# Performance work log

Measured on AMD Instinct MI355X. Metric: run time of the kernel, lower is better.

Reference implementation:

```python
import jax, jax.numpy as jnp
import numpy as np

BETA = 0.25  # commitment cost


def setup_inputs() -> dict:
    key = jax.random.key(0)
    k1, k2 = jax.random.split(key)
    B, C, T = 16, 256, 1024      # batch, emb_dim channels, sequence length
    N_EMB = 8192                 # codebook size
    z = jax.random.normal(k1, (B, C, T), dtype=jnp.float32)
    # original init: uniform(-1/n_emb, 1/n_emb); scale a normal similarly small
    emb = jax.random.normal(k2, (N_EMB, C), dtype=jnp.float32) * (1.0 / N_EMB)
    return {"z": z, "emb": emb}


def reference(z, emb):
    sg = jax.lax.stop_gradient
    # [B, C, T] -> [B, T, C]
    zt = jnp.transpose(z, (0, 2, 1))
    B, T, C = zt.shape
    zf = zt.reshape(-1, C)  # [B*T, C]
    # squared euclidean distances: ||z||^2 + ||e||^2 - 2 z.e  -> [B*T, N]
    d = (jnp.sum(zf * zf, axis=1, keepdims=True)
         + jnp.sum(emb * emb, axis=1)
         - 2.0 * jnp.einsum('bd,nd->bn', zf, emb))
    idx = jnp.argmin(d, axis=-1)               # [B*T]
    z_q = emb[idx].reshape(B, T, C)            # [B, T, C]
    loss = (BETA * jnp.mean((sg(z_q) - zt) ** 2)
            + jnp.mean((z_q - sg(zt)) ** 2))
    # straight-through estimator
    z_q = zt + sg(z_q - zt)
    z_q = jnp.transpose(z_q, (0, 2, 1))        # back to [B, C, T]
    return z_q, loss, idx
```

## Files before the change

kernel.cpp:

```cpp
#include <hip/hip_runtime.h>


#define C_    256
#define T_    1024
#define M_    16384
#define N_    8192

#define OUT_ZQ   0
#define OUT_LOSS 4194304
#define OUT_IDX  4194305

#define WS_SZ    0
#define WS_SE    16384
#define WS_PART  24576
#define MIN_OFF  131072u
#define FB_OFF   8519680u
#define WS_NEED  16908288u
#define O_I1     24576
#define O_I2     40960
#define O_PART   73728

typedef __attribute__((ext_vector_type(8))) short bf16x8;
typedef __attribute__((ext_vector_type(4))) float f32x4;
typedef unsigned long long ull;

__device__ __forceinline__ unsigned short f2b(float f) {
    unsigned u = __float_as_uint(f);
    return (unsigned short)((u + 0x7FFFu + ((u >> 16) & 1u)) >> 16);
}
__device__ __forceinline__ float b2f(unsigned short u) {
    return __uint_as_float(((unsigned)u) << 16);
}

__global__ __launch_bounds__(256) void vq_sums(const float* __restrict__ z,
                                               const float* __restrict__ emb,
                                               float* __restrict__ ws) {
    int gid = blockIdx.x * 256 + threadIdx.x;
    if (gid < M_) {
        int b = gid >> 10, t = gid & (T_ - 1);
        const float* zp = z + (size_t)b * C_ * T_ + t;
        float blk[2];
#pragma unroll
        for (int h = 0; h < 2; ++h) {
            float r[8];
#pragma unroll
            for (int j = 0; j < 8; ++j) {
                float v = zp[(size_t)(h * 128 + j) * T_];
                r[j] = __fmul_rn(v, v);
            }
            for (int i = 8; i < 128; i += 8)
#pragma unroll
                for (int j = 0; j < 8; ++j) {
                    float v = zp[(size_t)(h * 128 + i + j) * T_];
                    r[j] = __fadd_rn(r[j], __fmul_rn(v, v));
                }
            blk[h] = __fadd_rn(__fadd_rn(__fadd_rn(r[0], r[1]), __fadd_rn(r[2], r[3])),
                               __fadd_rn(__fadd_rn(r[4], r[5]), __fadd_rn(r[6], r[7])));
        }
        ws[WS_SZ + gid] = __fadd_rn(blk[0], blk[1]);
    } else if (gid < M_ + N_) {
        int n = gid - M_;
        const float* ep = emb + (size_t)n * C_;
        float blk[2];
#pragma unroll
        for (int h = 0; h < 2; ++h) {
            float r[8];
#pragma unroll
            for (int j = 0; j < 8; ++j) {
                float v = ep[h * 128 + j];
                r[j] = __fmul_rn(v, v);
            }
            for (int i = 8; i < 128; i += 8)
#pragma unroll
                for (int j = 0; j < 8; ++j) {
                    float v = ep[h * 128 + i + j];
                    r[j] = __fadd_rn(r[j], __fmul_rn(v, v));
                }
            blk[h] = __fadd_rn(__fadd_rn(__fadd_rn(r[0], r[1]), __fadd_rn(r[2], r[3])),
                               __fadd_rn(__fadd_rn(r[4], r[5]), __fadd_rn(r[6], r[7])));
        }
        ws[WS_SE + n] = __fadd_rn(blk[0], blk[1]);
    }
}

__global__ __launch_bounds__(256) void vq_prep_b(const float* __restrict__ emb,
                                                 char* __restrict__ fb) {
    int gid = blockIdx.x * 256 + threadIdx.x;
    int n = gid >> 5, kg = gid & 31;
    const float* ep = emb + (size_t)n * C_ + kg * 8;
    unsigned hi[8], lo[8];
#pragma unroll
    for (int j = 0; j < 8; ++j) {
        float v = ep[j];
        unsigned short h = f2b(v);
        hi[j] = h;
        lo[j] = f2b(v - b2f(h));
    }
    int nt = n >> 4, kt = kg >> 2, lane = (kg & 3) * 16 + (n & 15);
    size_t base = ((size_t)((nt * 8 + kt) * 2) << 10) + (lane << 4);
    uint4 hv = {hi[0] | (hi[1] << 16), hi[2] | (hi[3] << 16), hi[4] | (hi[5] << 16), hi[6] | (hi[7] << 16)};
    uint4 lv = {lo[0] | (lo[1] << 16), lo[2] | (lo[3] << 16), lo[4] | (lo[5] << 16), lo[6] | (lo[7] << 16)};
    *(uint4*)(fb + base) = hv;
    *(uint4*)(fb + base + 1024) = lv;
}

__global__ __launch_bounds__(256, 2) void vq_mfma2(
        const float* __restrict__ z, const char* __restrict__ fb,
        const float* __restrict__ sz, const float* __restrict__ se,
        ull* __restrict__ minima) {
    __shared__ __align__(16) char ldsA[65536];
    __shared__ __align__(16) char ldsB[16384];

    const int tid = threadIdx.x;
    const int lane = tid & 63;
    const int w = tid >> 6, wm = w & 1, wn = w >> 1;
    const int quad = lane >> 4, li = lane & 15;
    const int mb = blockIdx.x, ns = blockIdx.y;

    {
        const float* zb = z + (size_t)(mb >> 4) * C_ * T_ + ((mb & 15) << 6);
#pragma unroll
        for (int p = 0; p < 4; ++p) {
            int c  = p * 64 + (tid >> 2);
            int tq = tid & 3;
            const float* src = zb + (size_t)c * T_ + tq * 16;
            int kt = c >> 5, kg3 = (c >> 3) & 3, j = c & 7;
            unsigned short* d0 = (unsigned short*)(ldsA + (((tq * 8 + kt) * 2 + 0) << 10) + (kg3 << 8) + (j << 1));
            unsigned short* d1 = (unsigned short*)(ldsA + (((tq * 8 + kt) * 2 + 1) << 10) + (kg3 << 8) + (j << 1));
#pragma unroll
            for (int u = 0; u < 4; ++u) {
                float4 v = *(const float4*)(src + u * 4);
                float vv[4] = {v.x, v.y, v.z, v.w};
#pragma unroll
                for (int e = 0; e < 4; ++e) {
                    unsigned short h = f2b(vv[e]);
                    unsigned short l = f2b(vv[e] - b2f(h));
                    int i = u * 4 + e;
                    d0[i * 8] = h;
                    d1[i * 8] = l;
                }
            }
        }
    }

    float szr[8];
#pragma unroll
    for (int mt = 0; mt < 2; ++mt)
#pragma unroll
        for (int r = 0; r < 4; ++r)
            szr[mt * 4 + r] = sz[(mb << 6) + (wm << 5) + (mt << 4) + (quad << 2) + r];

    ull key[8];
#pragma unroll
    for (int s = 0; s < 8; ++s) key[s] = ~0ULL;

    const int f = tid >> 4, pos = (tid & 15) << 4;

    for (int nt = 0; nt < 32; ++nt) {
        f32x4 acc[2][4];
#pragma unroll
        for (int i = 0; i < 2; ++i)
#pragma unroll
            for (int j = 0; j < 4; ++j) acc[i][j] = (f32x4){0.f, 0.f, 0.f, 0.f};
        const int ntile0 = ns * 256 + nt * 8;

        for (int kt = 0; kt < 8; ++kt) {
            __syncthreads();
            {
                const char* srcB = fb + ((((size_t)(ntile0 + (f >> 1)) * 8 + kt) * 2 + (f & 1)) << 10) + pos;
                char* dB = ldsB + (f << 10) + pos;
#pragma unroll
                for (int i = 0; i < 4; ++i)
                    *(uint4*)(dB + i * 256) = *(const uint4*)(srcB + i * 256);
            }
            __syncthreads();
            bf16x8 a[2][2];
#pragma unroll
            for (int mt = 0; mt < 2; ++mt) {
                a[mt][0] = *(const bf16x8*)(ldsA + ((((wm * 2 + mt) * 8 + kt) * 2 + 0) << 10) + (lane << 4));
                a[mt][1] = *(const bf16x8*)(ldsA + ((((wm * 2 + mt) * 8 + kt) * 2 + 1) << 10) + (lane << 4));
            }
#pragma unroll
            for (int nt4 = 0; nt4 < 4; ++nt4) {
                bf16x8 bh = *(const bf16x8*)(ldsB + ((((wn * 4 + nt4) * 2 + 0)) << 10) + (lane << 4));
                bf16x8 bl = *(const bf16x8*)(ldsB + ((((wn * 4 + nt4) * 2 + 1)) << 10) + (lane << 4));
#pragma unroll
                for (int mt = 0; mt < 2; ++mt) {
                    f32x4 c = acc[mt][nt4];
                    c = __builtin_amdgcn_mfma_f32_16x16x32_bf16(a[mt][0], bh, c, 0, 0, 0);
                    c = __builtin_amdgcn_mfma_f32_16x16x32_bf16(a[mt][0], bl, c, 0, 0, 0);
                    c = __builtin_amdgcn_mfma_f32_16x16x32_bf16(a[mt][1], bh, c, 0, 0, 0);
                    acc[mt][nt4] = c;
                }
            }
        }
#pragma unroll
        for (int nt4 = 0; nt4 < 4; ++nt4) {
            const int ncol = ns * 4096 + nt * 128 + (wn * 4 + nt4) * 16 + li;
            const float sev = se[ncol];
#pragma unroll
            for (int mt = 0; mt < 2; ++mt) {
                f32x4 c = acc[mt][nt4];
#pragma unroll
                for (int r = 0; r < 4; ++r) {
                    float s = fmaf(-2.f, c[r], __fadd_rn(szr[mt * 4 + r], sev));
                    ull k = ((ull)__float_as_uint(s) << 32) | (unsigned)ncol;
                    int sl = mt * 4 + r;
                    if (k < key[sl]) key[sl] = k;
                }
            }
        }
        if (nt & 1) {
            int sc = nt >> 1;
#pragma unroll
            for (int sl = 0; sl < 8; ++sl) {
                ull kk = key[sl];
#pragma unroll
                for (int off = 1; off <= 8; off <<= 1) {
                    ull o = __shfl_xor(kk, off, 64);
                    if (o < kk) kk = o;
                }
                if (li == 0) {
                    int row = (mb << 6) + (wm << 5) + ((sl >> 2) << 4) + (quad << 2) + (sl & 3);
                    minima[(size_t)row * 64 + ((ns * 16 + sc) * 2 + wn)] = kk;
                }
                key[sl] = ~0ULL;
            }
        }
    }
}

__global__ __launch_bounds__(256) void vq_pick2(
        const float* __restrict__ z, const float* __restrict__ emb,
        const float* __restrict__ ws, const ull* __restrict__ minima,
        float* __restrict__ out) {
    __shared__ float Lz[256 * 17];
    const float* sz = ws + WS_SZ;
    const float* se = ws + WS_SE;
    const int tid = threadIdx.x;
    const int w = tid >> 6, lane = tid & 63, li = lane & 15;
    const int m0 = blockIdx.x * 16;
    const int b = m0 >> 10, t0 = m0 & (T_ - 1);

    {
        const float* src = z + (size_t)b * C_ * T_ + (size_t)tid * T_ + t0;
#pragma unroll
        for (int u = 0; u < 4; ++u) {
            float4 v = *(const float4*)(src + u * 4);
            Lz[tid * 17 + u * 4 + 0] = v.x;
            Lz[tid * 17 + u * 4 + 1] = v.y;
            Lz[tid * 17 + u * 4 + 2] = v.z;
            Lz[tid * 17 + u * 4 + 3] = v.w;
        }
    }
    __syncthreads();

    for (int rr = 0; rr < 4; ++rr) {
        const int tloc = w * 4 + rr;
        const int m = m0 + tloc;
        ull kmin = minima[(size_t)m * 64 + lane];
        int cand[4];
#pragma unroll
        for (int rep = 0; rep < 4; ++rep) {
            ull bf = kmin;
#pragma unroll
            for (int off = 1; off <= 32; off <<= 1) {
                ull o = __shfl_xor(bf, off, 64);
                if (o < bf) bf = o;
            }
            int ix = (int)(unsigned)(bf & 0xFFFFFFFFull);
            cand[rep] = ix < 0 ? 0 : (ix > N_ - 1 ? N_ - 1 : ix);
            if (kmin == bf) kmin = ~0ULL;
        }
        const int cn = cand[lane >> 4];
        const float* ep = emb + (size_t)cn * C_;
        double sum = 0.0;
#pragma unroll
        for (int cc = 0; cc < 16; ++cc) {
            int c = cc * 16 + li;
            sum = fma((double)Lz[c * 17 + tloc], (double)ep[c], sum);
        }
#pragma unroll
        for (int off = 1; off <= 8; off <<= 1)
            sum += __shfl_xor(sum, off, 64);
        double s0 = __shfl(sum, 0, 64), s1 = __shfl(sum, 16, 64);
        double s2 = __shfl(sum, 32, 64), s3 = __shfl(sum, 48, 64);
        if (lane == 0) {
            float szm = sz[m];
            float d0 = fmaf(-2.f, (float)s0, __fadd_rn(szm, se[cand[0]]));
            float d1 = fmaf(-2.f, (float)s1, __fadd_rn(szm, se[cand[1]]));
            float d2 = fmaf(-2.f, (float)s2, __fadd_rn(szm, se[cand[2]]));
            float d3 = fmaf(-2.f, (float)s3, __fadd_rn(szm, se[cand[3]]));
            float bd = d0; int bi = cand[0];
            if (d1 < bd || (d1 == bd && cand[1] < bi)) { bd = d1; bi = cand[1]; }
            if (d2 < bd || (d2 == bd && cand[2] < bi)) { bd = d2; bi = cand[2]; }
            if (d3 < bd || (d3 == bd && cand[3] < bi)) { bd = d3; bi = cand[3]; }
            out[OUT_IDX + m] = (float)bi;
        }
    }
}

__global__ __launch_bounds__(256) void vq_pass1_fp32(
        const float* __restrict__ z,
        const float* __restrict__ emb,
        float* __restrict__ ws) {
    __shared__ float As[32][68];
    __shared__ float Bs[32][68];
    const float* s_z = ws + WS_SZ;
    const float* s_e = ws + WS_SE;
    int* i1ws = (int*)ws + O_I1;
    int* i2ws = (int*)ws + O_I2;
    const int tid = threadIdx.x;
    const int mt  = blockIdx.x;
    const int tx  = tid & 15, ty = tid >> 4;
    const int b   = mt >> 4;
    const int t0  = (mt << 6) & (T_ - 1);
    const float* zbase = z + (size_t)b * C_ * T_ + t0;
    const int a_k = tid >> 4;
    const int a_m = (tid & 15) << 2;
    const int b_j = tid >> 2;
    const int b_q = (tid & 3) << 3;
    const float4 sz4 = *(const float4*)(s_z + mt * 64 + (ty << 2));
    const float szv[4] = {sz4.x, sz4.y, sz4.z, sz4.w};
    float v1[4], v2[4];
    int   i1[4], i2[4];
#pragma unroll
    for (int i = 0; i < 4; ++i) {
        v1[i] = INFINITY; v2[i] = INFINITY;
        i1[i] = 0x7FFFFFFF; i2[i] = 0x7FFFFFFF;
    }
    for (int nt = 0; nt < N_ / 64; ++nt) {
        const int n0 = nt * 64;
        float acc[4][4];
#pragma unroll
        for (int i = 0; i < 4; ++i)
#pragma unroll
            for (int j = 0; j < 4; ++j) acc[i][j] = 0.f;
        for (int kt = 0; kt < C_; kt += 32) {
            __syncthreads();
#pragma unroll
            for (int p = 0; p < 2; ++p) {
                int k = a_k + p * 16;
                float4 af = *(const float4*)(zbase + (size_t)(kt + k) * T_ + a_m);
                *(float4*)&As[k][a_m] = af;
            }
            {
                const float* ep = emb + (size_t)(n0 + b_j) * C_ + kt + b_q;
                float4 e0 = ((const float4*)ep)[0];
                float4 e1 = ((const float4*)ep)[1];
                Bs[b_q + 0][b_j] = e0.x; Bs[b_q + 1][b_j] = e0.y;
                Bs[b_q + 2][b_j] = e0.z; Bs[b_q + 3][b_j] = e0.w;
                Bs[b_q + 4][b_j] = e1.x; Bs[b_q + 5][b_j] = e1.y;
                Bs[b_q + 6][b_j] = e1.z; Bs[b_q + 7][b_j] = e1.w;
            }
            __syncthreads();
#pragma unroll
            for (int k = 0; k < 32; ++k) {
                const float4 a  = *(const float4*)&As[k][ty << 2];
                const float4 bv = *(const float4*)&Bs[k][tx << 2];
                acc[0][0] = fmaf(a.x, bv.x, acc[0][0]);
                acc[0][1] = fmaf(a.x, bv.y, acc[0][1]);
                acc[0][2] = fmaf(a.x, bv.z, acc[0][2]);
                acc[0][3] = fmaf(a.x, bv.w, acc[0][3]);
                acc[1][0] = fmaf(a.y, bv.x, acc[1][0]);
                acc[1][1] = fmaf(a.y, bv.y, acc[1][1]);
                acc[1][2] = fmaf(a.y, bv.z, acc[1][2]);
                acc[1][3] = fmaf(a.y, bv.w, acc[1][3]);
                acc[2][0] = fmaf(a.z, bv.x, acc[2][0]);
                acc[2][1] = fmaf(a.z, bv.y, acc[2][1]);
                acc[2][2] = fmaf(a.z, bv.z, acc[2][2]);
                acc[2][3] = fmaf(a.z, bv.w, acc[2][3]);
                acc[3][0] = fmaf(a.w, bv.x, acc[3][0]);
                acc[3][1] = fmaf(a.w, bv.y, acc[3][1]);
                acc[3][2] = fmaf(a.w, bv.z, acc[3][2]);
                acc[3][3] = fmaf(a.w, bv.w, acc[3][3]);
            }
        }
        const float4 se4 = *(const float4*)(s_e + n0 + (tx << 2));
        const float sev[4] = {se4.x, se4.y, se4.z, se4.w};
#pragma unroll
        for (int j = 0; j < 4; ++j) {
            const int n = n0 + (tx << 2) + j;
#pragma unroll
            for (int i = 0; i < 4; ++i) {
                float A = __fadd_rn(szv[i], sev[j]);
                float s = fmaf(-2.f, acc[i][j], A);
                if (s < v1[i]) { v2[i] = v1[i]; i2[i] = i1[i]; v1[i] = s; i1[i] = n; }
                else if (s < v2[i]) { v2[i] = s; i2[i] = n; }
            }
        }
    }
#pragma unroll
    for (int i = 0; i < 4; ++i) {
        float a1 = v1[i], a2 = v2[i];
        int   y1 = i1[i], y2 = i2[i];
#pragma unroll
        for (int off = 8; off >= 1; off >>= 1) {
            float o1 = __shfl_xor(a1, off, 64); int p1 = __shfl_xor(y1, off, 64);
            float o2 = __shfl_xor(a2, off, 64); int p2 = __shfl_xor(y2, off, 64);
            bool alt = (o1 < a1) || (o1 == a1 && p1 < y1);
            float w1 = alt ? o1 : a1; int q1 = alt ? p1 : y1;
            float lv = alt ? a1 : o1; int lq = alt ? y1 : p1;
            float wv = alt ? o2 : a2; int wq = alt ? p2 : y2;
            bool sb = (lv < wv) || (lv == wv && lq < wq);
            a2 = sb ? lv : wv; y2 = sb ? lq : wq;
            a1 = w1; y1 = q1;
        }
        if (tx == 0) {
            int m = mt * 64 + (ty << 2) + i;
            i1ws[m] = y1;
            i2ws[m] = y2;
        }
    }
}

__global__ __launch_bounds__(256) void vq_pass2_fp32(
        const float* __restrict__ z,
        const float* __restrict__ emb,
        float* __restrict__ ws,
        float* __restrict__ out) {
    const float* s_z = ws + WS_SZ;
    const float* s_e = ws + WS_SE;
    const int* i1ws = (const int*)ws + O_I1;
    const int* i2ws = (const int*)ws + O_I2;
    const int tid  = threadIdx.x;
    const int wave = tid >> 6, lane = tid & 63;
    const int half = lane >> 5;
    const int c0   = (lane & 31) << 3;
    const int rowbase = (blockIdx.x * 4 + wave) * 64;
    for (int r = 0; r < 64; ++r) {
        const int m = rowbase + r;
        int c1 = i1ws[m], c2 = i2ws[m];
        c1 = c1 < 0 ? 0 : (c1 > N_ - 1 ? N_ - 1 : c1);
        c2 = c2 < 0 ? 0 : (c2 > N_ - 1 ? N_ - 1 : c2);
        const int b = m >> 10, t = m & (T_ - 1);
        const float* zp = z + (size_t)b * C_ * T_ + t;
        const int cand = half ? c2 : c1;
        const float* ep = emb + (size_t)cand * C_;
        double sum = 0.0;
#pragma unroll
        for (int c = 0; c < 8; ++c)
            sum = fma((double)zp[(size_t)(c0 + c) * T_], (double)ep[c0 + c], sum);
#pragma unroll
        for (int off = 1; off <= 16; off <<= 1)
            sum += __shfl_xor(sum, off, 64);
        double s1 = __shfl(sum, 0, 64);
        double s2 = __shfl(sum, 32, 64);
        if (lane == 0) {
            float p1 = (float)s1, p2 = (float)s2;
            float d1 = fmaf(-2.f, p1, __fadd_rn(s_z[m], s_e[c1]));
            float d2 = fmaf(-2.f, p2, __fadd_rn(s_z[m], s_e[c2]));
            int win = ((d2 < d1) || (d2 == d1 && c2 < c1)) ? c2 : c1;
            out[OUT_IDX + m] = (float)win;
        }
    }
}

__global__ __launch_bounds__(256) void vq_gather(
        const float* __restrict__ z,
        const float* __restrict__ emb,
        float* __restrict__ partial,
        float* __restrict__ out) {
    __shared__ float Ls[64][129];
    __shared__ int   idxs[64];
    __shared__ float wred[4];
    const int tid = threadIdx.x;
    const int mg  = blockIdx.x;
    const int m0  = mg << 6;
    const int b   = m0 >> 10;
    const int t0  = m0 & (T_ - 1);
    if (tid < 64) {
        int ix = (int)out[OUT_IDX + m0 + tid];
        idxs[tid] = ix < 0 ? 0 : (ix > N_ - 1 ? N_ - 1 : ix);
    }
    __syncthreads();
    float lsum = 0.f;
    const int w = tid >> 6, l = tid & 63;
    const int tt2 = tid & 63, c0 = tid >> 6;
    const size_t base = (size_t)b * (C_ * T_) + t0 + tt2;
#pragma unroll
    for (int ch = 0; ch < 2; ++ch) {
        __syncthreads();
#pragma unroll
        for (int it = 0; it < 8; ++it) {
            int tt = it * 8 + w * 2 + (l >> 5);
            int cq = l & 31;
            int row = idxs[tt];
            float4 ev = *(const float4*)(emb + (size_t)row * C_ + ch * 128 + (cq << 2));
            Ls[tt][(cq << 2) + 0] = ev.x;
            Ls[tt][(cq << 2) + 1] = ev.y;
            Ls[tt][(cq << 2) + 2] = ev.z;
            Ls[tt][(cq << 2) + 3] = ev.w;
        }
        __syncthreads();
#pragma unroll
        for (int st = 0; st < 32; ++st) {
            int c_l = (st << 2) + c0;
            int c   = (ch << 7) + c_l;
            float v = Ls[tt2][c_l];
            size_t off = base + (size_t)c * T_;
            out[OUT_ZQ + off] = v;
            float d = v - z[off];
            lsum = fmaf(d, d, lsum);
        }
    }
#pragma unroll
    for (int off = 32; off >= 1; off >>= 1) lsum += __shfl_xor(lsum, off, 64);
    if (l == 0) wred[w] = lsum;
    __syncthreads();
    if (tid == 0) partial[mg] = wred[0] + wred[1] + wred[2] + wred[3];
}

__global__ __launch_bounds__(256) void vq_loss(const float* __restrict__ partial,
                                               float* __restrict__ out) {
    __shared__ float wred[4];
    const int tid = threadIdx.x;
    float v = partial[tid];
#pragma unroll
    for (int off = 32; off >= 1; off >>= 1) v += __shfl_xor(v, off, 64);
    if ((tid & 63) == 0) wred[tid >> 6] = v;
    __syncthreads();
    if (tid == 0)
        out[OUT_LOSS] = (wred[0] + wred[1] + wred[2] + wred[3]) * (1.25f / 4194304.f);
}

extern "C" void kernel_launch(void* const* d_in, const int* in_sizes, int n_in,
                              void* d_out, int out_size, void* d_ws, size_t ws_size,
                              hipStream_t stream) {
    const float* z   = (const float*)d_in[0];
    const float* emb = (const float*)d_in[1];
    float* out = (float*)d_out;
    float* ws  = (float*)d_ws;

    vq_sums<<<dim3((M_ + N_) / 256), dim3(256), 0, stream>>>(z, emb, ws);

    if (ws_size >= WS_NEED) {
        char* fb = (char*)d_ws + FB_OFF;
        ull* minima = (ull*)((char*)d_ws + MIN_OFF);
        vq_prep_b<<<dim3(1024), dim3(256), 0, stream>>>(emb, fb);
        vq_mfma2<<<dim3(256, 2), dim3(256), 0, stream>>>(z, fb, ws + WS_SZ, ws + WS_SE, minima);
        vq_pick2<<<dim3(1024), dim3(256), 0, stream>>>(z, emb, ws, minima, out);
        vq_gather<<<dim3(M_ / 64), dim3(256), 0, stream>>>(z, emb, ws + WS_PART, out);
        vq_loss<<<dim3(1), dim3(256), 0, stream>>>(ws + WS_PART, out);
    } else {
        vq_pass1_fp32<<<dim3(M_ / 64), dim3(256), 0, stream>>>(z, emb, ws);
        vq_pass2_fp32<<<dim3(64), dim3(256), 0, stream>>>(z, emb, ws, out);
        vq_gather<<<dim3(M_ / 64), dim3(256), 0, stream>>>(z, emb, ws + O_PART, out);
        vq_loss<<<dim3(1), dim3(256), 0, stream>>>(ws + O_PART, out);
    }
}
```

Before: 369.8 us.

## Stream B fragments from global into registers with prefetch, drop LDS B staging

The MFMA kernel no longer stages codebook tiles through shared memory with two barriers per k-step. Each wave now loads its B fragments directly from global into registers and prefetches the next k-step while computing. Each wave covers all 64 rows and two 16-column tiles, so the minima cells are reorganised. The two prep kernels are also merged into one launch. This trades LDS traffic and synchronisation for more global and L2 loads per wave and more registers (16 keys and 16 row sums), which may reduce occupancy. The fallback path now launches the merged prep and uses WS_PART where it previously used O_PART, which could break the fallback if those workspace regions overlap.

New measurement: 568.2 us. +53.6%, slower.

```diff
diff --git a/kernel.cpp b/kernel.cpp
--- a/kernel.cpp
+++ b/kernel.cpp
@@ -32,88 +32,88 @@
     return __uint_as_float(((unsigned)u) << 16);
 }
 
-__global__ __launch_bounds__(256) void vq_sums(const float* __restrict__ z,
+__global__ __launch_bounds__(256) void vq_prep(const float* __restrict__ z,
                                                const float* __restrict__ emb,
-                                               float* __restrict__ ws) {
-    int gid = blockIdx.x * 256 + threadIdx.x;
-    if (gid < M_) {
-        int b = gid >> 10, t = gid & (T_ - 1);
-        const float* zp = z + (size_t)b * C_ * T_ + t;
-        float blk[2];
-#pragma unroll
-        for (int h = 0; h < 2; ++h) {
-            float r[8];
-#pragma unroll
-            for (int j = 0; j < 8; ++j) {
-                float v = zp[(size_t)(h * 128 + j) * T_];
-                r[j] = __fmul_rn(v, v);
-            }
-            for (int i = 8; i < 128; i += 8)
+                                               float* __restrict__ ws,
+                                               char* __restrict__ fb) {
+    const int tid = threadIdx.x;
+    if (blockIdx.x < 1024) {
+        int gid = blockIdx.x * 256 + tid;
+        int n = gid >> 5, kg = gid & 31;
+        const float* ep = emb + (size_t)n * C_ + kg * 8;
+        unsigned hi[8], lo[8];
+#pragma unroll
+        for (int j = 0; j < 8; ++j) {
+            float v = ep[j];
+            unsigned short h = f2b(v);
+            hi[j] = h;
+            lo[j] = f2b(v - b2f(h));
+        }
+        int nt = n >> 4, kt = kg >> 2, lane = (kg & 3) * 16 + (n & 15);
+        size_t base = ((size_t)((nt * 8 + kt) * 2) << 10) + (lane << 4);
+        uint4 hv = {hi[0] | (hi[1] << 16), hi[2] | (hi[3] << 16), hi[4] | (hi[5] << 16), hi[6] | (hi[7] << 16)};
+        uint4 lv = {lo[0] | (lo[1] << 16), lo[2] | (lo[3] << 16), lo[4] | (lo[5] << 16), lo[6] | (lo[7] << 16)};
+        *(uint4*)(fb + base) = hv;
+        *(uint4*)(fb + base + 1024) = lv;
+    } else {
+        int gid = (blockIdx.x - 1024) * 256 + tid;
+        if (gid < M_) {
+            int b = gid >> 10, t = gid & (T_ - 1);
+            const float* zp = z + (size_t)b * C_ * T_ + t;
+            float blk[2];
+#pragma unroll
+            for (int h = 0; h < 2; ++h) {
+                float r[8];
 #pragma unroll
                 for (int j = 0; j < 8; ++j) {
-                    float v = zp[(size_t)(h * 128 + i + j) * T_];
-                    r[j] = __fadd_rn(r[j], __fmul_rn(v, v));
-                }
-            blk[h] = __fadd_rn(__fadd_rn(__fadd_rn(r[0], r[1]), __fadd_rn(r[2], r[3])),
-                               __fadd_rn(__fadd_rn(r[4], r[5]), __fadd_rn(r[6], r[7])));
-        }
-        ws[WS_SZ + gid] = __fadd_rn(blk[0], blk[1]);
-    } else if (gid < M_ + N_) {
-        int n = gid - M_;
-        const float* ep = emb + (size_t)n * C_;
-        float blk[2];
-#pragma unroll
-        for (int h = 0; h < 2; ++h) {
-            float r[8];
-#pragma unroll
-            for (int j = 0; j < 8; ++j) {
-                float v = ep[h * 128 + j];
-                r[j] = __fmul_rn(v, v);
-            }
-            for (int i = 8; i < 128; i += 8)
+                    float v = zp[(size_t)(h * 128 + j) * T_];
+                    r[j] = __fmul_rn(v, v);
+                }
+                for (int i = 8; i < 128; i += 8)
+#pragma unroll
+                    for (int j = 0; j < 8; ++j) {
+                        float v = zp[(size_t)(h * 128 + i + j) * T_];
+                        r[j] = __fadd_rn(r[j], __fmul_rn(v, v));
+                    }
+                blk[h] = __fadd_rn(__fadd_rn(__fadd_rn(r[0], r[1]), __fadd_rn(r[2], r[3])),
+                                   __fadd_rn(__fadd_rn(r[4], r[5]), __fadd_rn(r[6], r[7])));
+            }
+            ws[WS_SZ + gid] = __fadd_rn(blk[0], blk[1]);
+        } else if (gid < M_ + N_) {
+            int n = gid - M_;
+            const float* ep = emb + (size_t)n * C_;
+            float blk[2];
+#pragma unroll
+            for (int h = 0; h < 2; ++h) {
+                float r[8];
 #pragma unroll
                 for (int j = 0; j < 8; ++j) {
-                    float v = ep[h * 128 + i + j];
-                    r[j] = __fadd_rn(r[j], __fmul_rn(v, v));
-                }
-            blk[h] = __fadd_rn(__fadd_rn(__fadd_rn(r[0], r[1]), __fadd_rn(r[2], r[3])),
-                               __fadd_rn(__fadd_rn(r[4], r[5]), __fadd_rn(r[6], r[7])));
-        }
-        ws[WS_SE + n] = __fadd_rn(blk[0], blk[1]);
-    }
-}
-
-__global__ __launch_bounds__(256) void vq_prep_b(const float* __restrict__ emb,
-                                                 char* __restrict__ fb) {
-    int gid = blockIdx.x * 256 + threadIdx.x;
-    int n = gid >> 5, kg = gid & 31;
-    const float* ep = emb + (size_t)n * C_ + kg * 8;
-    unsigned hi[8], lo[8];
-#pragma unroll
-    for (int j = 0; j < 8; ++j) {
-        float v = ep[j];
-        unsigned short h = f2b(v);
-        hi[j] = h;
-        lo[j] = f2b(v - b2f(h));
-    }
-    int nt = n >> 4, kt = kg >> 2, lane = (kg & 3) * 16 + (n & 15);
-    size_t base = ((size_t)((nt * 8 + kt) * 2) << 10) + (lane << 4);
-    uint4 hv = {hi[0] | (hi[1] << 16), hi[2] | (hi[3] << 16), hi[4] | (hi[5] << 16), hi[6] | (hi[7] << 16)};
-    uint4 lv = {lo[0] | (lo[1] << 16), lo[2] | (lo[3] << 16), lo[4] | (lo[5] << 16), lo[6] | (lo[7] << 16)};
-    *(uint4*)(fb + base) = hv;
-    *(uint4*)(fb + base + 1024) = lv;
-}
-
-__global__ __launch_bounds__(256, 2) void vq_mfma2(
+                    float v = ep[h * 128 + j];
+                    r[j] = __fmul_rn(v, v);
+                }
+                for (int i = 8; i < 128; i += 8)
+#pragma unroll
+                    for (int j = 0; j < 8; ++j) {
+                        float v = ep[h * 128 + i + j];
+                        r[j] = __fadd_rn(r[j], __fmul_rn(v, v));
+                    }
+                blk[h] = __fadd_rn(__fadd_rn(__fadd_rn(r[0], r[1]), __fadd_rn(r[2], r[3])),
+                                   __fadd_rn(__fadd_rn(r[4], r[5]), __fadd_rn(r[6], r[7])));
+            }
+            ws[WS_SE + n] = __fadd_rn(blk[0], blk[1]);
+        }
+    }
+}
+
+__global__ __launch_bounds__(256, 2) void vq_mfma3(
         const float* __restrict__ z, const char* __restrict__ fb,
         const float* __restrict__ sz, const float* __restrict__ se,
         ull* __restrict__ minima) {
     __shared__ __align__(16) char ldsA[65536];
-    __shared__ __align__(16) char ldsB[16384];
 
     const int tid = threadIdx.x;
     const int lane = tid & 63;
-    const int w = tid >> 6, wm = w & 1, wn = w >> 1;
+    const int wn = tid >> 6;
     const int quad = lane >> 4, li = lane & 15;
     const int mb = blockIdx.x, ns = blockIdx.y;
 
@@ -142,50 +142,54 @@
             }
         }
     }
-
-    float szr[8];
-#pragma unroll
-    for (int mt = 0; mt < 2; ++mt)
+    __syncthreads();
+
+    float szr[16];
+#pragma unroll
+    for (int mt = 0; mt < 4; ++mt)
 #pragma unroll
         for (int r = 0; r < 4; ++r)
-            szr[mt * 4 + r] = sz[(mb << 6) + (wm << 5) + (mt << 4) + (quad << 2) + r];
-
-    ull key[8];
-#pragma unroll
-    for (int s = 0; s < 8; ++s) key[s] = ~0ULL;
-
-    const int f = tid >> 4, pos = (tid & 15) << 4;
+            szr[mt * 4 + r] = sz[(mb << 6) + (mt << 4) + (quad << 2) + r];
+
+    ull key[16];
+#pragma unroll
+    for (int s = 0; s < 16; ++s) key[s] = ~0ULL;
+
+    const char* fbl = fb + (lane << 4);
+#define BPTR(nt_, kt_, q_) ((const bf16x8*)(fbl + \
+        ((((size_t)(ns * 256 + (nt_) * 8 + wn * 2 + ((q_) >> 1)) * 8 + (kt_)) * 2 + ((q_) & 1)) << 10)))
+
+    bf16x8 bcur[4];
+#pragma unroll
+    for (int q = 0; q < 4; ++q) bcur[q] = *BPTR(0, 0, q);
 
     for (int nt = 0; nt < 32; ++nt) {
-        f32x4 acc[2][4];
-#pragma unroll
-        for (int i = 0; i < 2; ++i)
-#pragma unroll
-            for (int j = 0; j < 4; ++j) acc[i][j] = (f32x4){0.f, 0.f, 0.f, 0.f};
-        const int ntile0 = ns * 256 + nt * 8;
-
+        f32x4 acc[4][2];
+#pragma unroll
+        for (int i = 0; i < 4; ++i)
+#pragma unroll
+            for (int j = 0; j < 2; ++j) acc[i][j] = (f32x4){0.f, 0.f, 0.f, 0.f};
+
+#pragma unroll
         for (int kt = 0; kt < 8; ++kt) {
-            __syncthreads();
-            {
-                const char* srcB = fb + ((((size_t)(ntile0 + (f >> 1)) * 8 + kt) * 2 + (f & 1)) << 10) + pos;
-                char* dB = ldsB + (f << 10) + pos;
-#pragma unroll
-                for (int i = 0; i < 4; ++i)
-                    *(uint4*)(dB + i * 256) = *(const uint4*)(srcB + i * 256);
-            }
-            __syncthreads();
-            bf16x8 a[2][2];
-#pragma unroll
-            for (int mt = 0; mt < 2; ++mt) {
-                a[mt][0] = *(const bf16x8*)(ldsA + ((((wm * 2 + mt) * 8 + kt) * 2 + 0) << 10) + (lane << 4));
-                a[mt][1] = *(const bf16x8*)(ldsA + ((((wm * 2 + mt) * 8 + kt) * 2 + 1) << 10) + (lane << 4));
-            }
-#pragma unroll
-            for (int nt4 = 0; nt4 < 4; ++nt4) {
-                bf16x8 bh = *(const bf16x8*)(ldsB + ((((wn * 4 + nt4) * 2 + 0)) << 10) + (lane << 4));
-                bf16x8 bl = *(const bf16x8*)(ldsB + ((((wn * 4 + nt4) * 2 + 1)) << 10) + (lane << 4));
-#pragma unroll
-                for (int mt = 0; mt < 2; ++mt) {
+            bf16x8 bnext[4];
+            const int pnt = (kt == 7) ? ((nt + 1) & 31) : nt;
+            const int pkt = (kt + 1) & 7;
+#pragma unroll
+            for (int q = 0; q < 4; ++q) bnext[q] = *BPTR(pnt, pkt, q);
+
+            bf16x8 a[4][2];
+#pragma unroll
+            for (int mt = 0; mt < 4; ++mt) {
+                a[mt][0] = *(const bf16x8*)(ldsA + (((mt * 8 + kt) * 2 + 0) << 10) + (lane << 4));
+                a[mt][1] = *(const bf16x8*)(ldsA + (((mt * 8 + kt) * 2 + 1) << 10) + (lane << 4));
+            }
+#pragma unroll
+            for (int nt4 = 0; nt4 < 2; ++nt4) {
+                const bf16x8 bh = bcur[nt4 * 2 + 0];
+                const bf16x8 bl = bcur[nt4 * 2 + 1];
+#pragma unroll
+                for (int mt = 0; mt < 4; ++mt) {
                     f32x4 c = acc[mt][nt4];
                     c = __builtin_amdgcn_mfma_f32_16x16x32_bf16(a[mt][0], bh, c, 0, 0, 0);
                     c = __builtin_amdgcn_mfma_f32_16x16x32_bf16(a[mt][0], bl, c, 0, 0, 0);
@@ -193,27 +197,30 @@
                     acc[mt][nt4] = c;
                 }
             }
-        }
-#pragma unroll
-        for (int nt4 = 0; nt4 < 4; ++nt4) {
-            const int ncol = ns * 4096 + nt * 128 + (wn * 4 + nt4) * 16 + li;
+#pragma unroll
+            for (int q = 0; q < 4; ++q) bcur[q] = bnext[q];
+        }
+
+#pragma unroll
+        for (int nt4 = 0; nt4 < 2; ++nt4) {
+            const int ncol = ((ns * 256 + nt * 8 + wn * 2 + nt4) << 4) + li;
             const float sev = se[ncol];
 #pragma unroll
-            for (int mt = 0; mt < 2; ++mt) {
+            for (int mt = 0; mt < 4; ++mt) {
                 f32x4 c = acc[mt][nt4];
 #pragma unroll
                 for (int r = 0; r < 4; ++r) {
                     float s = fmaf(-2.f, c[r], __fadd_rn(szr[mt * 4 + r], sev));
                     ull k = ((ull)__float_as_uint(s) << 32) | (unsigned)ncol;
-                    int sl = mt * 4 + r;
+                    const int sl = mt * 4 + r;
                     if (k < key[sl]) key[sl] = k;
                 }
             }
         }
-        if (nt & 1) {
-            int sc = nt >> 1;
-#pragma unroll
-            for (int sl = 0; sl < 8; ++sl) {
+        if ((nt & 3) == 3) {
+            const int cell = ns * 32 + (nt >> 2) * 4 + wn;
+#pragma unroll
+            for (int sl = 0; sl < 16; ++sl) {
                 ull kk = key[sl];
 #pragma unroll
                 for (int off = 1; off <= 8; off <<= 1) {
@@ -221,13 +228,14 @@
                     if (o < kk) kk = o;
                 }
                 if (li == 0) {
-                    int row = (mb << 6) + (wm << 5) + ((sl >> 2) << 4) + (quad << 2) + (sl & 3);
-                    minima[(size_t)row * 64 + ((ns * 16 + sc) * 2 + wn)] = kk;
+                    int row = (mb << 6) + ((sl >> 2) << 4) + (quad << 2) + (sl & 3);
+                    minima[(size_t)row * 64 + cell] = kk;
                 }
                 key[sl] = ~0ULL;
             }
         }
     }
+#undef BPTR
 }
 
 __global__ __launch_bounds__(256) void vq_pick2(
@@ -532,20 +540,19 @@
     float* out = (float*)d_out;
     float* ws  = (float*)d_ws;
 
-    vq_sums<<<dim3((M_ + N_) / 256), dim3(256), 0, stream>>>(z, emb, ws);
-
     if (ws_size >= WS_NEED) {
         char* fb = (char*)d_ws + FB_OFF;
         ull* minima = (ull*)((char*)d_ws + MIN_OFF);
-        vq_prep_b<<<dim3(1024), dim3(256), 0, stream>>>(emb, fb);
-        vq_mfma2<<<dim3(256, 2), dim3(256), 0, stream>>>(z, fb, ws + WS_SZ, ws + WS_SE, minima);
+        vq_prep<<<dim3(1024 + (M_ + N_) / 256), dim3(256), 0, stream>>>(z, emb, ws, fb);
+        vq_mfma3<<<dim3(256, 2), dim3(256), 0, stream>>>(z, fb, ws + WS_SZ, ws + WS_SE, minima);
         vq_pick2<<<dim3(1024), dim3(256), 0, stream>>>(z, emb, ws, minima, out);
         vq_gather<<<dim3(M_ / 64), dim3(256), 0, stream>>>(z, emb, ws + WS_PART, out);
         vq_loss<<<dim3(1), dim3(256), 0, stream>>>(ws + WS_PART, out);
     } else {
+        vq_prep<<<dim3(1024 + (M_ + N_) / 256), dim3(256), 0, stream>>>(z, emb, ws, (char*)d_ws + (ws_size > FB_OFF ? FB_OFF : 0));
         vq_pass1_fp32<<<dim3(M_ / 64), dim3(256), 0, stream>>>(z, emb, ws);
         vq_pass2_fp32<<<dim3(64), dim3(256), 0, stream>>>(z, emb, ws, out);
-        vq_gather<<<dim3(M_ / 64), dim3(256), 0, stream>>>(z, emb, ws + O_PART, out);
-        vq_loss<<<dim3(1), dim3(256), 0, stream>>>(ws + O_PART, out);
-    }
-}
+        vq_gather<<<dim3(M_ / 64), dim3(256), 0, stream>>>(z, emb, ws + WS_PART, out);
+        vq_loss<<<dim3(1), dim3(256), 0, stream>>>(ws + WS_PART, out);
+    }
+}
```

## Restructure distance GEMM with 32x32 MFMA, async LDS prefetch, fused prep kernel

Applied to the files above, without the earlier changes.

Replaces the 16x16x32 MFMA distance kernel with a 512-thread, one-block-per-64-rows kernel that uses 32x32x16 bf16 MFMAs. Each block walks the full codebook and double-buffers B tiles in LDS through global_load_lds, so the next tile loads while the current one is computed. The sums kernel and the emb bf16 split are fused into a single prep launch, and the candidate-minima layout widens to 128 cells per row, with the pick kernel updated to match. The intent is higher MFMA throughput and hidden global-load latency, at the cost of larger LDS use, one block per CU, and a larger workspace requirement.

Result: slower. 519.9 us (+40.6%).

```diff
diff --git a/kernel.cpp b/kernel.cpp
--- a/kernel.cpp
+++ b/kernel.cpp
@@ -14,14 +14,14 @@
 #define WS_SE    16384
 #define WS_PART  24576
 #define MIN_OFF  131072u
-#define FB_OFF   8519680u
-#define WS_NEED  16908288u
+#define FB_OFF   16908288u
+#define WS_NEED  25296896u
 #define O_I1     24576
 #define O_I2     40960
 #define O_PART   73728
 
-typedef __attribute__((ext_vector_type(8))) short bf16x8;
-typedef __attribute__((ext_vector_type(4))) float f32x4;
+typedef __attribute__((ext_vector_type(8)))  short bf16x8;
+typedef __attribute__((ext_vector_type(16))) float f32x16;
 typedef unsigned long long ull;
 
 __device__ __forceinline__ unsigned short f2b(float f) {
@@ -30,6 +30,11 @@
 }
 __device__ __forceinline__ float b2f(unsigned short u) {
     return __uint_as_float(((unsigned)u) << 16);
+}
+__device__ __forceinline__ void gl_lds16(const void* g, void* l) {
+    __builtin_amdgcn_global_load_lds(
+        (const __attribute__((address_space(1))) unsigned int*)g,
+        (__attribute__((address_space(3))) unsigned int*)l, 16, 0, 0);
 }
 
 __global__ __launch_bounds__(256) void vq_sums(const float* __restrict__ z,
@@ -83,150 +88,219 @@
     }
 }
 
-__global__ __launch_bounds__(256) void vq_prep_b(const float* __restrict__ emb,
-                                                 char* __restrict__ fb) {
-    int gid = blockIdx.x * 256 + threadIdx.x;
-    int n = gid >> 5, kg = gid & 31;
-    const float* ep = emb + (size_t)n * C_ + kg * 8;
-    unsigned hi[8], lo[8];
-#pragma unroll
-    for (int j = 0; j < 8; ++j) {
-        float v = ep[j];
-        unsigned short h = f2b(v);
-        hi[j] = h;
-        lo[j] = f2b(v - b2f(h));
-    }
-    int nt = n >> 4, kt = kg >> 2, lane = (kg & 3) * 16 + (n & 15);
-    size_t base = ((size_t)((nt * 8 + kt) * 2) << 10) + (lane << 4);
-    uint4 hv = {hi[0] | (hi[1] << 16), hi[2] | (hi[3] << 16), hi[4] | (hi[5] << 16), hi[6] | (hi[7] << 16)};
-    uint4 lv = {lo[0] | (lo[1] << 16), lo[2] | (lo[3] << 16), lo[4] | (lo[5] << 16), lo[6] | (lo[7] << 16)};
-    *(uint4*)(fb + base) = hv;
-    *(uint4*)(fb + base + 1024) = lv;
-}
-
-__global__ __launch_bounds__(256, 2) void vq_mfma2(
+__global__ __launch_bounds__(256) void vq_prep(const float* __restrict__ z,
+                                               const float* __restrict__ emb,
+                                               float* __restrict__ ws,
+                                               char* __restrict__ fb) {
+    const int tid = threadIdx.x;
+    if (blockIdx.x < 1024) {
+        int gid = blockIdx.x * 256 + tid;
+        int n = gid >> 5, kg = gid & 31;
+        const float* ep = emb + (size_t)n * C_ + kg * 8;
+        unsigned hi[8], lo[8];
+#pragma unroll
+        for (int j = 0; j < 8; ++j) {
+            float v = ep[j];
+            unsigned short h = f2b(v);
+            hi[j] = h;
+            lo[j] = f2b(v - b2f(h));
+        }
+        int gnb = n >> 5, k16 = kg >> 1, k8 = kg & 1;
+        int lanep = (n & 31) + (k8 << 5);
+        size_t base = ((size_t)((gnb * 16 + k16) * 2) << 10) + (lanep << 4);
+        uint4 hv = {hi[0] | (hi[1] << 16), hi[2] | (hi[3] << 16), hi[4] | (hi[5] << 16), hi[6] | (hi[7] << 16)};
+        uint4 lv = {lo[0] | (lo[1] << 16), lo[2] | (lo[3] << 16), lo[4] | (lo[5] << 16), lo[6] | (lo[7] << 16)};
+        *(uint4*)(fb + base) = hv;
+        *(uint4*)(fb + base + 1024) = lv;
+    } else {
+        int gid = (blockIdx.x - 1024) * 256 + tid;
+        if (gid < M_) {
+            int b = gid >> 10, t = gid & (T_ - 1);
+            const float* zp = z + (size_t)b * C_ * T_ + t;
+            float blk[2];
+#pragma unroll
+            for (int h = 0; h < 2; ++h) {
+                float r[8];
+#pragma unroll
+                for (int j = 0; j < 8; ++j) {
+                    float v = zp[(size_t)(h * 128 + j) * T_];
+                    r[j] = __fmul_rn(v, v);
+                }
+                for (int i = 8; i < 128; i += 8)
+#pragma unroll
+                    for (int j = 0; j < 8; ++j) {
+                        float v = zp[(size_t)(h * 128 + i + j) * T_];
+                        r[j] = __fadd_rn(r[j], __fmul_rn(v, v));
+                    }
+                blk[h] = __fadd_rn(__fadd_rn(__fadd_rn(r[0], r[1]), __fadd_rn(r[2], r[3])),
+                                   __fadd_rn(__fadd_rn(r[4], r[5]), __fadd_rn(r[6], r[7])));
+            }
+            ws[WS_SZ + gid] = __fadd_rn(blk[0], blk[1]);
+        } else if (gid < M_ + N_) {
+            int n = gid - M_;
+            const float* ep = emb + (size_t)n * C_;
+            float blk[2];
+#pragma unroll
+            for (int h = 0; h < 2; ++h) {
+                float r[8];
+#pragma unroll
+                for (int j = 0; j < 8; ++j) {
+                    float v = ep[h * 128 + j];
+                    r[j] = __fmul_rn(v, v);
+                }
+                for (int i = 8; i < 128; i += 8)
+#pragma unroll
+                    for (int j = 0; j < 8; ++j) {
+                        float v = ep[h * 128 + i + j];
+                        r[j] = __fadd_rn(r[j], __fmul_rn(v, v));
+                    }
+                blk[h] = __fadd_rn(__fadd_rn(__fadd_rn(r[0], r[1]), __fadd_rn(r[2], r[3])),
+                                   __fadd_rn(__fadd_rn(r[4], r[5]), __fadd_rn(r[6], r[7])));
+            }
+            ws[WS_SE + n] = __fadd_rn(blk[0], blk[1]);
+        }
+    }
+}
+
+__global__ __launch_bounds__(512, 1) void vq_mfma4(
         const float* __restrict__ z, const char* __restrict__ fb,
         const float* __restrict__ sz, const float* __restrict__ se,
         ull* __restrict__ minima) {
     __shared__ __align__(16) char ldsA[65536];
-    __shared__ __align__(16) char ldsB[16384];
+    __shared__ __align__(16) char ldsB[65536];
 
     const int tid = threadIdx.x;
     const int lane = tid & 63;
-    const int w = tid >> 6, wm = w & 1, wn = w >> 1;
-    const int quad = lane >> 4, li = lane & 15;
-    const int mb = blockIdx.x, ns = blockIdx.y;
+    const int w = tid >> 6;
+    const int mb = blockIdx.x;
 
     {
         const float* zb = z + (size_t)(mb >> 4) * C_ * T_ + ((mb & 15) << 6);
-#pragma unroll
-        for (int p = 0; p < 4; ++p) {
-            int c  = p * 64 + (tid >> 2);
-            int tq = tid & 3;
-            const float* src = zb + (size_t)c * T_ + tq * 16;
-            int kt = c >> 5, kg3 = (c >> 3) & 3, j = c & 7;
-            unsigned short* d0 = (unsigned short*)(ldsA + (((tq * 8 + kt) * 2 + 0) << 10) + (kg3 << 8) + (j << 1));
-            unsigned short* d1 = (unsigned short*)(ldsA + (((tq * 8 + kt) * 2 + 1) << 10) + (kg3 << 8) + (j << 1));
-#pragma unroll
-            for (int u = 0; u < 4; ++u) {
-                float4 v = *(const float4*)(src + u * 4);
-                float vv[4] = {v.x, v.y, v.z, v.w};
-#pragma unroll
-                for (int e = 0; e < 4; ++e) {
-                    unsigned short h = f2b(vv[e]);
-                    unsigned short l = f2b(vv[e] - b2f(h));
-                    int i = u * 4 + e;
-                    d0[i * 8] = h;
-                    d1[i * 8] = l;
-                }
-            }
-        }
-    }
-
-    float szr[8];
+        const int m = tid & 63, co = tid >> 6;
+#pragma unroll
+        for (int r = 0; r < 4; ++r) {
+            const int c_oct = r * 8 + co;
+            const int k16 = c_oct >> 1, k8 = c_oct & 1;
+            const int lanep = (m & 31) + (k8 << 5);
+            const int mt = m >> 5;
+            unsigned hi[8], lo[8];
+#pragma unroll
+            for (int j = 0; j < 8; ++j) {
+                float v = zb[(size_t)(c_oct * 8 + j) * T_ + m];
+                unsigned short h = f2b(v);
+                hi[j] = h;
+                lo[j] = f2b(v - b2f(h));
+            }
+            size_t base = ((size_t)((mt * 16 + k16) * 2) << 10) + (lanep << 4);
+            uint4 hv = {hi[0] | (hi[1] << 16), hi[2] | (hi[3] << 16), hi[4] | (hi[5] << 16), hi[6] | (hi[7] << 16)};
+            uint4 lv = {lo[0] | (lo[1] << 16), lo[2] | (lo[3] << 16), lo[4] | (lo[5] << 16), lo[6] | (lo[7] << 16)};
+            *(uint4*)(ldsA + base) = hv;
+            *(uint4*)(ldsA + base + 1024) = lv;
+        }
+    }
+
+    float szr[32];
 #pragma unroll
     for (int mt = 0; mt < 2; ++mt)
 #pragma unroll
-        for (int r = 0; r < 4; ++r)
-            szr[mt * 4 + r] = sz[(mb << 6) + (wm << 5) + (mt << 4) + (quad << 2) + r];
-
-    ull key[8];
-#pragma unroll
-    for (int s = 0; s < 8; ++s) key[s] = ~0ULL;
-
-    const int f = tid >> 4, pos = (tid & 15) << 4;
-
-    for (int nt = 0; nt < 32; ++nt) {
-        f32x4 acc[2][4];
-#pragma unroll
-        for (int i = 0; i < 2; ++i)
-#pragma unroll
-            for (int j = 0; j < 4; ++j) acc[i][j] = (f32x4){0.f, 0.f, 0.f, 0.f};
-        const int ntile0 = ns * 256 + nt * 8;
-
-        for (int kt = 0; kt < 8; ++kt) {
-            __syncthreads();
-            {
-                const char* srcB = fb + ((((size_t)(ntile0 + (f >> 1)) * 8 + kt) * 2 + (f & 1)) << 10) + pos;
-                char* dB = ldsB + (f << 10) + pos;
-#pragma unroll
-                for (int i = 0; i < 4; ++i)
-                    *(uint4*)(dB + i * 256) = *(const uint4*)(srcB + i * 256);
-            }
-            __syncthreads();
-            bf16x8 a[2][2];
+        for (int r = 0; r < 16; ++r)
+            szr[mt * 16 + r] = sz[(mb << 6) + mt * 32 + (r & 3) + 8 * (r >> 2) + 4 * (lane >> 5)];
+
+    ull key[32];
+#pragma unroll
+    for (int s = 0; s < 32; ++s) key[s] = ~0ULL;
+
+    {
+#pragma unroll
+        for (int i = 0; i < 4; ++i) {
+            const int p = w * 4 + i, nb = p >> 1, h = p & 1;
+            const size_t src = ((((size_t)(0 * 128 + 0 * 16 + nb) * 16 + 0) * 2 + h) << 10) + (lane << 4);
+            gl_lds16(fb + src, ldsB + (p << 10));
+        }
+    }
+    __syncthreads();
+
+    f32x16 acc[2][2];
+    for (int s = 0; s < 256; ++s) {
+        const int ns = s >> 7, nt = (s >> 4) & 7, kt = s & 15;
+        {
+            const int pn = (s + 1 < 256) ? s + 1 : 255;
+            const int pns = pn >> 7, pnt = (pn >> 4) & 7, pkt = pn & 15;
+            const int buf = (s + 1) & 1;
+#pragma unroll
+            for (int i = 0; i < 4; ++i) {
+                const int p = w * 4 + i, nb = p >> 1, h = p & 1;
+                const size_t src = ((((size_t)(pns * 128 + pnt * 16 + nb) * 16 + pkt) * 2 + h) << 10) + (lane << 4);
+                gl_lds16(fb + src, ldsB + buf * 32768 + (p << 10));
+            }
+        }
+        if (kt == 0) {
+#pragma unroll
+            for (int i = 0; i < 2; ++i)
+#pragma unroll
+                for (int j = 0; j < 2; ++j)
+#pragma unroll
+                    for (int r = 0; r < 16; ++r) acc[i][j][r] = 0.f;
+        }
+        {
+            const char* bbase = ldsB + (s & 1) * 32768;
+            bf16x8 ah[2], al[2], bh[2], bl[2];
 #pragma unroll
             for (int mt = 0; mt < 2; ++mt) {
-                a[mt][0] = *(const bf16x8*)(ldsA + ((((wm * 2 + mt) * 8 + kt) * 2 + 0) << 10) + (lane << 4));
-                a[mt][1] = *(const bf16x8*)(ldsA + ((((wm * 2 + mt) * 8 + kt) * 2 + 1) << 10) + (lane << 4));
-            }
-#pragma unroll
-            for (int nt4 = 0; nt4 < 4; ++nt4) {
-                bf16x8 bh = *(const bf16x8*)(ldsB + ((((wn * 4 + nt4) * 2 + 0)) << 10) + (lane << 4));
-                bf16x8 bl = *(const bf16x8*)(ldsB + ((((wn * 4 + nt4) * 2 + 1)) << 10) + (lane << 4));
+                ah[mt] = *(const bf16x8*)(ldsA + (((mt * 16 + kt) * 2 + 0) << 10) + (lane << 4));
+                al[mt] = *(const bf16x8*)(ldsA + (((mt * 16 + kt) * 2 + 1) << 10) + (lane << 4));
+            }
+#pragma unroll
+            for (int nb = 0; nb < 2; ++nb) {
+                bh[nb] = *(const bf16x8*)(bbase + (((w * 2 + nb) * 2 + 0) << 10) + (lane << 4));
+                bl[nb] = *(const bf16x8*)(bbase + (((w * 2 + nb) * 2 + 1) << 10) + (lane << 4));
+            }
+#pragma unroll
+            for (int nb = 0; nb < 2; ++nb)
 #pragma unroll
                 for (int mt = 0; mt < 2; ++mt) {
-                    f32x4 c = acc[mt][nt4];
-                    c = __builtin_amdgcn_mfma_f32_16x16x32_bf16(a[mt][0], bh, c, 0, 0, 0);
-                    c = __builtin_amdgcn_mfma_f32_16x16x32_bf16(a[mt][0], bl, c, 0, 0, 0);
-                    c = __builtin_amdgcn_mfma_f32_16x16x32_bf16(a[mt][1], bh, c, 0, 0, 0);
-                    acc[mt][nt4] = c;
-                }
-            }
-        }
-#pragma unroll
-        for (int nt4 = 0; nt4 < 4; ++nt4) {
-            const int ncol = ns * 4096 + nt * 128 + (wn * 4 + nt4) * 16 + li;
-            const float sev = se[ncol];
-#pragma unroll
-            for (int mt = 0; mt < 2; ++mt) {
-                f32x4 c = acc[mt][nt4];
-#pragma unroll
-                for (int r = 0; r < 4; ++r) {
-                    float s = fmaf(-2.f, c[r], __fadd_rn(szr[mt * 4 + r], sev));
-                    ull k = ((ull)__float_as_uint(s) << 32) | (unsigned)ncol;
-                    int sl = mt * 4 + r;
-                    if (k < key[sl]) key[sl] = k;
-                }
-            }
-        }
-        if (nt & 1) {
-            int sc = nt >> 1;
-#pragma unroll
-            for (int sl = 0; sl < 8; ++sl) {
+                    f32x16 c = acc[mt][nb];
+                    c = __builtin_amdgcn_mfma_f32_32x32x16_bf16(ah[mt], bh[nb], c, 0, 0, 0);
+                    c = __builtin_amdgcn_mfma_f32_32x32x16_bf16(ah[mt], bl[nb], c, 0, 0, 0);
+                    c = __builtin_amdgcn_mfma_f32_32x32x16_bf16(al[mt], bh[nb], c, 0, 0, 0);
+                    acc[mt][nb] = c;
+                }
+        }
+        if (kt == 15) {
+#pragma unroll
+            for (int nb = 0; nb < 2; ++nb) {
+                const int ncol = ns * 4096 + nt * 512 + (w * 2 + nb) * 32 + (lane & 31);
+                const float sev = se[ncol];
+#pragma unroll
+                for (int mt = 0; mt < 2; ++mt) {
+                    f32x16 c = acc[mt][nb];
+#pragma unroll
+                    for (int r = 0; r < 16; ++r) {
+                        float sc = fmaf(-2.f, c[r], __fadd_rn(szr[mt * 16 + r], sev));
+                        ull k = ((ull)__float_as_uint(sc) << 32) | (unsigned)ncol;
+                        const int sl = mt * 16 + r;
+                        if (k < key[sl]) key[sl] = k;
+                    }
+                }
+            }
+            const int cell = ns * 64 + nt * 8 + w;
+#pragma unroll
+            for (int sl = 0; sl < 32; ++sl) {
                 ull kk = key[sl];
 #pragma unroll
-                for (int off = 1; off <= 8; off <<= 1) {
+                for (int off = 1; off <= 16; off <<= 1) {
                     ull o = __shfl_xor(kk, off, 64);
                     if (o < kk) kk = o;
                 }
-                if (li == 0) {
-                    int row = (mb << 6) + (wm << 5) + ((sl >> 2) << 4) + (quad << 2) + (sl & 3);
-                    minima[(size_t)row * 64 + ((ns * 16 + sc) * 2 + wn)] = kk;
+                if ((lane & 31) == 0) {
+                    const int r = sl & 15;
+                    const int row = (mb << 6) + (sl >> 4) * 32 + (r & 3) + 8 * (r >> 2) + 4 * (lane >> 5);
+                    minima[(size_t)row * 128 + cell] = kk;
                 }
                 key[sl] = ~0ULL;
             }
         }
+        __syncthreads();
     }
 }
 
@@ -258,11 +332,12 @@
     for (int rr = 0; rr < 4; ++rr) {
         const int tloc = w * 4 + rr;
         const int m = m0 + tloc;
-        ull kmin = minima[(size_t)m * 64 + lane];
+        ull k0 = minima[(size_t)m * 128 + lane];
+        ull k1 = minima[(size_t)m * 128 + 64 + lane];
         int cand[4];
 #pragma unroll
         for (int rep = 0; rep < 4; ++rep) {
-            ull bf = kmin;
+            ull bf = k0 < k1 ? k0 : k1;
 #pragma unroll
             for (int off = 1; off <= 32; off <<= 1) {
                 ull o = __shfl_xor(bf, off, 64);
@@ -270,7 +345,8 @@
             }
             int ix = (int)(unsigned)(bf & 0xFFFFFFFFull);
             cand[rep] = ix < 0 ? 0 : (ix > N_ - 1 ? N_ - 1 : ix);
-            if (kmin == bf) kmin = ~0ULL;
+            if (k0 == bf) k0 = ~0ULL;
+            else if (k1 == bf) k1 = ~0ULL;
         }
         const int cn = cand[lane >> 4];
         const float* ep = emb + (size_t)cn * C_;
@@ -532,17 +608,16 @@
     float* out = (float*)d_out;
     float* ws  = (float*)d_ws;
 
-    vq_sums<<<dim3((M_ + N_) / 256), dim3(256), 0, stream>>>(z, emb, ws);
-
     if (ws_size >= WS_NEED) {
         char* fb = (char*)d_ws + FB_OFF;
         ull* minima = (ull*)((char*)d_ws + MIN_OFF);
-        vq_prep_b<<<dim3(1024), dim3(256), 0, stream>>>(emb, fb);
-        vq_mfma2<<<dim3(256, 2), dim3(256), 0, stream>>>(z, fb, ws + WS_SZ, ws + WS_SE, minima);
+        vq_prep<<<dim3(1024 + (M_ + N_) / 256), dim3(256), 0, stream>>>(z, emb, ws, fb);
+        vq_mfma4<<<dim3(256), dim3(512), 0, stream>>>(z, fb, ws + WS_SZ, ws + WS_SE, minima);
         vq_pick2<<<dim3(1024), dim3(256), 0, stream>>>(z, emb, ws, minima, out);
         vq_gather<<<dim3(M_ / 64), dim3(256), 0, stream>>>(z, emb, ws + WS_PART, out);
         vq_loss<<<dim3(1), dim3(256), 0, stream>>>(ws + WS_PART, out);
     } else {
+        vq_sums<<<dim3((M_ + N_) / 256), dim3(256), 0, stream>>>(z, emb, ws);
         vq_pass1_fp32<<<dim3(M_ / 64), dim3(256), 0, stream>>>(z, emb, ws);
         vq_pass2_fp32<<<dim3(64), dim3(256), 0, stream>>>(z, emb, ws, out);
         vq_gather<<<dim3(M_ / 64), dim3(256), 0, stream>>>(z, emb, ws + O_PART, out);
```
